# Kernel optimization log

Measured on AMD Instinct MI355X. Metric: run time of the kernel, lower is better.

## Reference

```python
import jax, jax.numpy as jnp
import numpy as np

N = 100000   # n_nodes
E = 600000   # n_edges
H = 128      # hidden_dim
D1 = H // 2  # GAT hidden channels


def gat_conv(h_in, src, dst, W, a_src, a_dst, b, n):
    """Single-head PyG GATConv with default add_self_loops=True, negative_slope=0.2."""
    h = h_in @ W.T                                   # [n, out]
    sl = jnp.arange(n)
    s = jnp.concatenate([src, sl])                   # self loops appended
    d = jnp.concatenate([dst, sl])
    alpha_s = (h * a_src).sum(-1)                    # [n]
    alpha_d = (h * a_dst).sum(-1)                    # [n]
    e = jax.nn.leaky_relu(alpha_s[s] + alpha_d[d], 0.2)   # [E+n]
    m = jax.ops.segment_max(e, d, num_segments=n)    # per-dst max (stable softmax)
    w = jnp.exp(e - m[d])
    z = jax.ops.segment_sum(w, d, num_segments=n)
    attn = w / z[d]                                  # segment softmax over incoming edges
    out = jax.ops.segment_sum(attn[:, None] * h[s], d, num_segments=n)
    return out + b


def setup_inputs() -> dict:
    key = jax.random.key(0)
    ks = jax.random.split(key, 14)
    sc = 0.2
    return {
        "x": jax.random.normal(ks[0], (N, 1), jnp.float32),
        "edge_index": jax.random.randint(ks[1], (2, E), 0, N, dtype=jnp.int64),
        # GAT layer 1: 1 -> 64
        "W_gat1": jax.random.normal(ks[2], (D1, 1), jnp.float32) * sc,
        "a_src1": jax.random.normal(ks[3], (D1,), jnp.float32) * sc,
        "a_dst1": jax.random.normal(ks[4], (D1,), jnp.float32) * sc,
        "b_gat1": jnp.zeros((D1,), jnp.float32),
        # GAT layer 2: 64 -> 128
        "W_gat2": jax.random.normal(ks[5], (H, D1), jnp.float32) * sc,
        "a_src2": jax.random.normal(ks[6], (H,), jnp.float32) * sc,
        "a_dst2": jax.random.normal(ks[7], (H,), jnp.float32) * sc,
        "b_gat2": jnp.zeros((H,), jnp.float32),
        # linear1: 1 -> 128, linear2: 128 -> 128
        "W_lin1": jax.random.normal(ks[8], (H, 1), jnp.float32) * sc,
        "b_lin1": jnp.zeros((H,), jnp.float32),
        "W_lin2": jax.random.normal(ks[9], (H, H), jnp.float32) * (sc / np.sqrt(H)),
        "b_lin2": jnp.zeros((H,), jnp.float32),
    }


def reference(x, edge_index, W_gat1, a_src1, a_dst1, b_gat1,
              W_gat2, a_src2, a_dst2, b_gat2,
              W_lin1, b_lin1, W_lin2, b_lin2):
    src, dst = edge_index[0], edge_index[1]
    n = x.shape[0]
    # GAT stack (2 layers, ReLU between, none after last — PyG GAT default act)
    h = gat_conv(x, src, dst, W_gat1, a_src1, a_dst1, b_gat1, n)
    h = jax.nn.relu(h)
    h = gat_conv(h, src, dst, W_gat2, a_src2, a_dst2, b_gat2, n)   # [n, 128]
    x1 = h @ W_lin2.T + b_lin2
    x2 = x @ W_lin1.T + b_lin1
    return x2 + jax.nn.relu(x1)
```

## Files before the change

kernel.cpp:

```cpp
#include <hip/hip_runtime.h>
#include <hip/hip_fp16.h>
#include <math.h>

#define LRELU(v) ((v) > 0.f ? (v) : 0.2f * (v))
#define SLOT_STRIDE 32

using short8 = __attribute__((ext_vector_type(8))) short;
using f32x4  = __attribute__((ext_vector_type(4))) float;

__device__ __forceinline__ unsigned int f2bf(float f) {
    unsigned int u = __float_as_uint(f);
    u += 0x7fffu + ((u >> 16) & 1u);
    return u >> 16;
}

#define C_VAS 4
#define C_VAD 68
#define C_BC 132
#define C_WCT 260

__global__ void k0_precompute(const float* W1, const float* as1, const float* ad1,
                              const float* W2, const float* as2, const float* ad2,
                              const float* b2, const float* Wl2, const float* bl2,
                              float* consts, unsigned short* Whc, int* cnt, int N) {
    int b = blockIdx.x, t = threadIdx.x;
    if (b < 64) {
        float acc = 0.f;
#pragma unroll 8
        for (int j = 0; j < 128; ++j) acc += Wl2[t * 128 + j] * W2[j * 64 + b];
        consts[C_WCT + b * 128 + t] = acc;
        Whc[t * 64 + b] = (unsigned short)f2bf(acc);
    } else if (b == 64) {
        if (t < 64) {
            float vs = 0.f, vd = 0.f;
            for (int c = 0; c < 128; ++c) {
                float w = W2[c * 64 + t];
                vs += as2[c] * w;
                vd += ad2[c] * w;
            }
            consts[C_VAS + t] = vs;
            consts[C_VAD + t] = vd;
        }
        float acc = bl2[t];
        for (int j = 0; j < 128; ++j) acc += Wl2[t * 128 + j] * b2[j];
        consts[C_BC + t] = acc;
        if (t < 64) {
            float p = W1[t] * as1[t], q = W1[t] * ad1[t];
#pragma unroll
            for (int m = 1; m < 64; m <<= 1) { p += __shfl_xor(p, m); q += __shfl_xor(q, m); }
            if (t == 0) { consts[0] = p; consts[1] = q; }
        }
    } else {
        int i = (b - 65) * 128 + t;
        if (i < N) cnt[i] = 0;
    }
}

__global__ void k_fill(const int* src, const int* dst, int* cnt, int* slots, int E) {
    int e = blockIdx.x * blockDim.x + threadIdx.x;
    if (e >= E) return;
    int d = dst[e];
    int pos = atomicAdd(&cnt[d], 1);
    if (pos < SLOT_STRIDE) slots[(size_t)d * SLOT_STRIDE + pos] = src[e];
}

__global__ void kL1(const float* x, const float* consts, const int* cnt, const int* slots,
                    const float* W1, const float* b1,
                    __half* hrelu, float* a2s, float* a2d, int N) {
    int lane = threadIdx.x;
    int grp = lane >> 4, c = lane & 15;
    int i = (blockIdx.x * blockDim.y + threadIdx.y) * 4 + grp;
    if (i >= N) return;
    float cs = consts[0], cd = consts[1];
    float xi = x[i];
    float w0 = __expf(LRELU(xi * (cs + cd)));
    int n = min(cnt[i], SLOT_STRIDE);
    float w = 0.f, wxl = 0.f;
    if (c < n) {
        int s = slots[(size_t)i * SLOT_STRIDE + c];
        float xs = x[s];
        float ww = __expf(LRELU(cs * xs + cd * xi));
        w = ww; wxl = ww * xs;
    }
    if (n > 16) {
        int l2 = 16 + c;
        if (l2 < n) {
            int s = slots[(size_t)i * SLOT_STRIDE + l2];
            float xs = x[s];
            float ww = __expf(LRELU(cs * xs + cd * xi));
            w += ww; wxl += ww * xs;
        }
    }
#pragma unroll
    for (int m = 1; m < 16; m <<= 1) {
        w   += __shfl_xor(w, m);
        wxl += __shfl_xor(wxl, m);
    }
    float a1 = (w0 * xi + wxl) / (w0 + w);
    float4 W4 = *(const float4*)(W1 + 4 * c);
    float4 B4 = *(const float4*)(b1 + 4 * c);
    float h0 = fmaxf(a1 * W4.x + B4.x, 0.f);
    float h1 = fmaxf(a1 * W4.y + B4.y, 0.f);
    float h2 = fmaxf(a1 * W4.z + B4.z, 0.f);
    float h3 = fmaxf(a1 * W4.w + B4.w, 0.f);
    __half2 p0 = __floats2half2_rn(h0, h1);
    __half2 p1 = __floats2half2_rn(h2, h3);
    uint2 st;
    st.x = *(unsigned int*)&p0;
    st.y = *(unsigned int*)&p1;
    *(uint2*)(hrelu + (size_t)i * 64 + 4 * c) = st;
    float4 vs = *(const float4*)(consts + C_VAS + 4 * c);
    float4 vd = *(const float4*)(consts + C_VAD + 4 * c);
    float ps = h0 * vs.x + h1 * vs.y + h2 * vs.z + h3 * vs.w;
    float pd = h0 * vd.x + h1 * vd.y + h2 * vd.z + h3 * vd.w;
#pragma unroll
    for (int m = 1; m < 16; m <<= 1) {
        ps += __shfl_xor(ps, m);
        pd += __shfl_xor(pd, m);
    }
    if (c == 0) { a2s[i] = ps; a2d[i] = pd; }
}

#define EDGE(sidx) do {                                                      \
    int _s = (sidx);                                                         \
    float _w = __expf(LRELU(a2s[_s] + adi));                                 \
    uint4 _r = *(const uint4*)(hrelu + (size_t)_s * 64 + 8 * c);             \
    float2 _q0 = __half22float2(*(const __half2*)&_r.x);                     \
    float2 _q1 = __half22float2(*(const __half2*)&_r.y);                     \
    float2 _q2 = __half22float2(*(const __half2*)&_r.z);                     \
    float2 _q3 = __half22float2(*(const __half2*)&_r.w);                     \
    a0 += _w * _q0.x; a1 += _w * _q0.y; a2 += _w * _q1.x; a3 += _w * _q1.y;  \
    a4 += _w * _q2.x; a5 += _w * _q2.y; a6 += _w * _q3.x; a7 += _w * _q3.y;  \
    z += _w; } while (0)

__global__ void kL2O(const float* x, const float* consts, const int* cnt, const int* slots,
                     const float* a2s, const float* a2d, const __half* hrelu,
                     const unsigned short* Whc, const float* Wl1, const float* bl1,
                     float* out, int N) {
    __shared__ unsigned short svh[64 * 72];
    int lane = threadIdx.x, wy = threadIdx.y;
    int tile = blockIdx.x * 64;
    int grp = lane >> 3, c = lane & 7;

#pragma unroll
    for (int pass = 0; pass < 2; ++pass) {
        int lr = wy * 16 + pass * 8 + grp;
        int i = tile + lr;
        if (i < N) {
            float adi = a2d[i];
            float w0 = __expf(LRELU(a2s[i] + adi));
            float z = w0;
            float a0, a1, a2, a3, a4, a5, a6, a7;
            {
                uint4 rs = *(const uint4*)(hrelu + (size_t)i * 64 + 8 * c);
                float2 p0 = __half22float2(*(const __half2*)&rs.x);
                float2 p1 = __half22float2(*(const __half2*)&rs.y);
                float2 p2 = __half22float2(*(const __half2*)&rs.z);
                float2 p3 = __half22float2(*(const __half2*)&rs.w);
                a0 = w0 * p0.x; a1 = w0 * p0.y; a2 = w0 * p1.x; a3 = w0 * p1.y;
                a4 = w0 * p2.x; a5 = w0 * p2.y; a6 = w0 * p3.x; a7 = w0 * p3.y;
            }
            const int4* sp4 = (const int4*)(slots + (size_t)i * SLOT_STRIDE);
            int n = min(cnt[i], SLOT_STRIDE);
            for (int b4 = 0; b4 < n; b4 += 4) {
                int4 s4 = sp4[b4 >> 2];
                int m = n - b4;
                if (m > 0) EDGE(s4.x);
                if (m > 1) EDGE(s4.y);
                if (m > 2) EDGE(s4.z);
                if (m > 3) EDGE(s4.w);
            }
            float inv = 1.f / z;
            uint4 o;
            o.x = f2bf(a0 * inv) | (f2bf(a1 * inv) << 16);
            o.y = f2bf(a2 * inv) | (f2bf(a3 * inv) << 16);
            o.z = f2bf(a4 * inv) | (f2bf(a5 * inv) << 16);
            o.w = f2bf(a6 * inv) | (f2bf(a7 * inv) << 16);
            *(uint4*)(&svh[lr * 72 + 8 * c]) = o;
        }
    }
    __syncthreads();

    int r = lane & 15, kg = lane >> 4;
    int lr = wy * 16 + r;
    int lrs = (tile + lr < N) ? lr : 0;
    short8 A0 = *(const short8*)(&svh[lrs * 72 + kg * 8]);
    short8 A1 = *(const short8*)(&svh[lrs * 72 + kg * 8 + 32]);

    f32x4 acc[8];
#pragma unroll
    for (int ct = 0; ct < 8; ++ct) {
        const unsigned short* bp = Whc + (ct * 16 + r) * 64 + kg * 8;
        short8 B0 = *(const short8*)bp;
        short8 B1 = *(const short8*)(bp + 32);
        f32x4 cacc = {0.f, 0.f, 0.f, 0.f};
        cacc = __builtin_amdgcn_mfma_f32_16x16x32_bf16(A0, B0, cacc, 0, 0, 0);
        cacc = __builtin_amdgcn_mfma_f32_16x16x32_bf16(A1, B1, cacc, 0, 0, 0);
        acc[ct] = cacc;
    }
    float xq[4];
#pragma unroll
    for (int q = 0; q < 4; ++q) {
        int node = tile + wy * 16 + kg * 4 + q;
        xq[q] = (node < N) ? x[node] : 0.f;
    }
#pragma unroll
    for (int ct = 0; ct < 8; ++ct) {
        int col = ct * 16 + r;
        float wl = Wl1[col], bl = bl1[col], bc = consts[C_BC + col];
#pragma unroll
        for (int q = 0; q < 4; ++q) {
            int node = tile + wy * 16 + kg * 4 + q;
            if (node < N)
                out[(size_t)node * 128 + col] = xq[q] * wl + bl + fmaxf(acc[ct][q] + bc, 0.f);
        }
    }
}

extern "C" void kernel_launch(void* const* d_in, const int* in_sizes, int n_in,
                              void* d_out, int out_size, void* d_ws, size_t ws_size,
                              hipStream_t stream) {
    const float* x   = (const float*)d_in[0];
    const int*   ei  = (const int*)d_in[1];
    const float* W1  = (const float*)d_in[2];
    const float* as1 = (const float*)d_in[3];
    const float* ad1 = (const float*)d_in[4];
    const float* b1  = (const float*)d_in[5];
    const float* W2  = (const float*)d_in[6];
    const float* as2 = (const float*)d_in[7];
    const float* ad2 = (const float*)d_in[8];
    const float* b2  = (const float*)d_in[9];
    const float* Wl1 = (const float*)d_in[10];
    const float* bl1 = (const float*)d_in[11];
    const float* Wl2 = (const float*)d_in[12];
    const float* bl2 = (const float*)d_in[13];

    int N = in_sizes[0];
    int E = in_sizes[1] / 2;
    const int* srcp = ei;
    const int* dstp = ei + E;

    float* ws = (float*)d_ws;
    float* consts = ws;
    int*   cnt    = (int*)(ws + 8704);
    int*   slots  = cnt + N;
    float* a2s    = (float*)(slots + (size_t)SLOT_STRIDE * N);
    float* a2d    = a2s + N;
    uintptr_t hb  = ((uintptr_t)(a2d + N) + 15) & ~(uintptr_t)15;
    __half* hrel  = (__half*)hb;
    unsigned short* Whc = (unsigned short*)(hrel + (size_t)64 * N);

    float* outp = (float*)d_out;

    dim3 b256(256);
    dim3 bw(64, 4);

    int zb = 65 + (N + 127) / 128;
    k0_precompute<<<zb, 128, 0, stream>>>(W1, as1, ad1, W2, as2, ad2, b2, Wl2, bl2,
                                          consts, Whc, cnt, N);
    k_fill<<<(E + 255) / 256, b256, 0, stream>>>(srcp, dstp, cnt, slots, E);
    kL1<<<(N + 15) / 16, bw, 0, stream>>>(x, consts, cnt, slots, W1, b1, hrel, a2s, a2d, N);
    kL2O<<<(N + 63) / 64, bw, 0, stream>>>(x, consts, cnt, slots, a2s, a2d, hrel,
                                           Whc, Wl1, bl1, outp, N);
}
```

Baseline: 96.10 us.

## Recompute layer-1 hidden features from scalar aggregate instead of storing 64-wide fp16 rows

Layer 1 has a 1-dim input, so each node's hidden vector is relu(a1*W1+b1) and is fully determined by the scalar aggregate a1. kL1 now stores only (a1, alpha_src) as a float2 per node. kL2O's edge gather loads 8 bytes per neighbor and rebuilds the 8-channel slice with FMAs and max, instead of reading a 128-byte fp16 row. This removes most of the random-gather memory traffic and the 12.8MB hrelu buffer, at the cost of extra ALU work per edge. It also skips the fp16 rounding of the hidden features.

```diff
diff --git a/kernel.cpp b/kernel.cpp
--- a/kernel.cpp
+++ b/kernel.cpp
@@ -66,7 +66,7 @@
 
 __global__ void kL1(const float* x, const float* consts, const int* cnt, const int* slots,
                     const float* W1, const float* b1,
-                    __half* hrelu, float* a2s, float* a2d, int N) {
+                    float2* pk, float* a2d, int N) {
     int lane = threadIdx.x;
     int grp = lane >> 4, c = lane & 15;
     int i = (blockIdx.x * blockDim.y + threadIdx.y) * 4 + grp;
@@ -103,12 +103,6 @@
     float h1 = fmaxf(a1 * W4.y + B4.y, 0.f);
     float h2 = fmaxf(a1 * W4.z + B4.z, 0.f);
     float h3 = fmaxf(a1 * W4.w + B4.w, 0.f);
-    __half2 p0 = __floats2half2_rn(h0, h1);
-    __half2 p1 = __floats2half2_rn(h2, h3);
-    uint2 st;
-    st.x = *(unsigned int*)&p0;
-    st.y = *(unsigned int*)&p1;
-    *(uint2*)(hrelu + (size_t)i * 64 + 4 * c) = st;
     float4 vs = *(const float4*)(consts + C_VAS + 4 * c);
     float4 vd = *(const float4*)(consts + C_VAD + 4 * c);
     float ps = h0 * vs.x + h1 * vs.y + h2 * vs.z + h3 * vs.w;
@@ -118,23 +112,24 @@
         ps += __shfl_xor(ps, m);
         pd += __shfl_xor(pd, m);
     }
-    if (c == 0) { a2s[i] = ps; a2d[i] = pd; }
-}
-
-#define EDGE(sidx) do {                                                      \
-    int _s = (sidx);                                                         \
-    float _w = __expf(LRELU(a2s[_s] + adi));                                 \
-    uint4 _r = *(const uint4*)(hrelu + (size_t)_s * 64 + 8 * c);             \
-    float2 _q0 = __half22float2(*(const __half2*)&_r.x);                     \
-    float2 _q1 = __half22float2(*(const __half2*)&_r.y);                     \
-    float2 _q2 = __half22float2(*(const __half2*)&_r.z);                     \
-    float2 _q3 = __half22float2(*(const __half2*)&_r.w);                     \
-    a0 += _w * _q0.x; a1 += _w * _q0.y; a2 += _w * _q1.x; a3 += _w * _q1.y;  \
-    a4 += _w * _q2.x; a5 += _w * _q2.y; a6 += _w * _q3.x; a7 += _w * _q3.y;  \
-    z += _w; } while (0)
+    if (c == 0) {
+        pk[i] = make_float2(a1, ps);
+        a2d[i] = pd;
+    }
+}
+
+#define EDGE(sidx) do {                                                       \
+    int _s = (sidx);                                                          \
+    float2 _p = pk[_s];                                                       \
+    float _w = __expf(LRELU(_p.y + adi));                                     \
+    z += _w;                                                                  \
+    _Pragma("unroll")                                                         \
+    for (int _j = 0; _j < 8; ++_j)                                            \
+        acc[_j] += _w * fmaxf(_p.x * W1f[_j] + b1f[_j], 0.f);                 \
+    } while (0)
 
 __global__ void kL2O(const float* x, const float* consts, const int* cnt, const int* slots,
-                     const float* a2s, const float* a2d, const __half* hrelu,
+                     const float2* pk, const float* a2d, const float* W1, const float* b1,
                      const unsigned short* Whc, const float* Wl1, const float* bl1,
                      float* out, int N) {
     __shared__ unsigned short svh[64 * 72];
@@ -142,24 +137,23 @@
     int tile = blockIdx.x * 64;
     int grp = lane >> 3, c = lane & 7;
 
+    float W1f[8], b1f[8];
+#pragma unroll
+    for (int j = 0; j < 8; ++j) { W1f[j] = W1[8 * c + j]; b1f[j] = b1[8 * c + j]; }
+
 #pragma unroll
     for (int pass = 0; pass < 2; ++pass) {
         int lr = wy * 16 + pass * 8 + grp;
         int i = tile + lr;
         if (i < N) {
             float adi = a2d[i];
-            float w0 = __expf(LRELU(a2s[i] + adi));
+            float2 pki = pk[i];
+            float w0 = __expf(LRELU(pki.y + adi));
             float z = w0;
-            float a0, a1, a2, a3, a4, a5, a6, a7;
-            {
-                uint4 rs = *(const uint4*)(hrelu + (size_t)i * 64 + 8 * c);
-                float2 p0 = __half22float2(*(const __half2*)&rs.x);
-                float2 p1 = __half22float2(*(const __half2*)&rs.y);
-                float2 p2 = __half22float2(*(const __half2*)&rs.z);
-                float2 p3 = __half22float2(*(const __half2*)&rs.w);
-                a0 = w0 * p0.x; a1 = w0 * p0.y; a2 = w0 * p1.x; a3 = w0 * p1.y;
-                a4 = w0 * p2.x; a5 = w0 * p2.y; a6 = w0 * p3.x; a7 = w0 * p3.y;
-            }
+            float acc[8];
+#pragma unroll
+            for (int j = 0; j < 8; ++j)
+                acc[j] = w0 * fmaxf(pki.x * W1f[j] + b1f[j], 0.f);
             const int4* sp4 = (const int4*)(slots + (size_t)i * SLOT_STRIDE);
             int n = min(cnt[i], SLOT_STRIDE);
             for (int b4 = 0; b4 < n; b4 += 4) {
@@ -172,10 +166,10 @@
             }
             float inv = 1.f / z;
             uint4 o;
-            o.x = f2bf(a0 * inv) | (f2bf(a1 * inv) << 16);
-            o.y = f2bf(a2 * inv) | (f2bf(a3 * inv) << 16);
-            o.z = f2bf(a4 * inv) | (f2bf(a5 * inv) << 16);
-            o.w = f2bf(a6 * inv) | (f2bf(a7 * inv) << 16);
+            o.x = f2bf(acc[0] * inv) | (f2bf(acc[1] * inv) << 16);
+            o.y = f2bf(acc[2] * inv) | (f2bf(acc[3] * inv) << 16);
+            o.z = f2bf(acc[4] * inv) | (f2bf(acc[5] * inv) << 16);
+            o.w = f2bf(acc[6] * inv) | (f2bf(acc[7] * inv) << 16);
             *(uint4*)(&svh[lr * 72 + 8 * c]) = o;
         }
     }
@@ -187,7 +181,7 @@
     short8 A0 = *(const short8*)(&svh[lrs * 72 + kg * 8]);
     short8 A1 = *(const short8*)(&svh[lrs * 72 + kg * 8 + 32]);
 
-    f32x4 acc[8];
+    f32x4 acc2[8];
 #pragma unroll
     for (int ct = 0; ct < 8; ++ct) {
         const unsigned short* bp = Whc + (ct * 16 + r) * 64 + kg * 8;
@@ -196,7 +190,7 @@
         f32x4 cacc = {0.f, 0.f, 0.f, 0.f};
         cacc = __builtin_amdgcn_mfma_f32_16x16x32_bf16(A0, B0, cacc, 0, 0, 0);
         cacc = __builtin_amdgcn_mfma_f32_16x16x32_bf16(A1, B1, cacc, 0, 0, 0);
-        acc[ct] = cacc;
+        acc2[ct] = cacc;
     }
     float xq[4];
 #pragma unroll
@@ -212,7 +206,7 @@
         for (int q = 0; q < 4; ++q) {
             int node = tile + wy * 16 + kg * 4 + q;
             if (node < N)
-                out[(size_t)node * 128 + col] = xq[q] * wl + bl + fmaxf(acc[ct][q] + bc, 0.f);
+                out[(size_t)node * 128 + col] = xq[q] * wl + bl + fmaxf(acc2[ct][q] + bc, 0.f);
         }
     }
 }
@@ -244,11 +238,9 @@
     float* consts = ws;
     int*   cnt    = (int*)(ws + 8704);
     int*   slots  = cnt + N;
-    float* a2s    = (float*)(slots + (size_t)SLOT_STRIDE * N);
-    float* a2d    = a2s + N;
-    uintptr_t hb  = ((uintptr_t)(a2d + N) + 15) & ~(uintptr_t)15;
-    __half* hrel  = (__half*)hb;
-    unsigned short* Whc = (unsigned short*)(hrel + (size_t)64 * N);
+    float2* pk    = (float2*)(slots + (size_t)SLOT_STRIDE * N);
+    float* a2d    = (float*)(pk + N);
+    unsigned short* Whc = (unsigned short*)(a2d + N);
 
     float* outp = (float*)d_out;
 
@@ -259,7 +251,7 @@
     k0_precompute<<<zb, 128, 0, stream>>>(W1, as1, ad1, W2, as2, ad2, b2, Wl2, bl2,
                                           consts, Whc, cnt, N);
     k_fill<<<(E + 255) / 256, b256, 0, stream>>>(srcp, dstp, cnt, slots, E);
-    kL1<<<(N + 15) / 16, bw, 0, stream>>>(x, consts, cnt, slots, W1, b1, hrel, a2s, a2d, N);
-    kL2O<<<(N + 63) / 64, bw, 0, stream>>>(x, consts, cnt, slots, a2s, a2d, hrel,
+    kL1<<<(N + 15) / 16, bw, 0, stream>>>(x, consts, cnt, slots, W1, b1, pk, a2d, N);
+    kL2O<<<(N + 63) / 64, bw, 0, stream>>>(x, consts, cnt, slots, pk, a2d, W1, b1,
                                            Whc, Wl1, bl1, outp, N);
 }
```

New measurement: 89.78 us. 6.6% less time.
